# Kernel optimization log

Measured on AMD Instinct MI355X. Metric: run time of the kernel, lower is better.

Reference implementation:

```python
import jax, jax.numpy as jnp
import numpy as np

# ---- static config (matches init_kwargs) ----
B, CIN, H, W = 32, 64, 32, 32
CO, K, G, PAD = 64, 7, 8, 3
R_RAMP = 3.0            # ramp size R
Z_INIT = 4.0            # initial adaptive-span value
MAXSZ = W // 2          # adaptive_mask max_size = image_size/2 = 16
CPG = CO // G           # channels per group


def _unfold(t, k):
    # torch x.unfold(2,k,1).unfold(3,k,1): [B,C,Hp,Wp] -> [B,C,Ho,Wo,kh,kw]
    ho = t.shape[2] - k + 1
    wo = t.shape[3] - k + 1
    return jnp.stack(
        [jnp.stack([t[:, :, i:i + ho, j:j + wo] for j in range(k)], axis=-1)
         for i in range(k)], axis=-2)


def _adaptive_mask(current_val):
    # AdaptiveMask.forward applied to [B,G,CPG,H,W]; x.shape[-1] == W.
    # one_d_mask[g, i] is the soft value written on 'ring' i (rows i and W-1-i,
    # columns spanning the ring interval) of a WxW mask.
    template = jnp.linspace(1.0 - MAXSZ, 0.0, MAXSZ)            # [MAXSZ]
    om = (template[None, :] + current_val * MAXSZ) / R_RAMP + 1.0
    om = jnp.clip(om, 0.0, 1.0)                                  # [G, MAXSZ]
    # (slice [-(W//2):] is identity since MAXSZ == W//2)
    i = jnp.arange(W)
    r = jnp.minimum(i, W - 1 - i)                                # ring index per row
    top = i <= (W - 1 - i)
    lo = jnp.where(top, r, r + 1)    # bottom row of ring misses its leftmost col
    hi = W - 1 - r
    c = jnp.arange(W)
    in_ring = (c[None, :] >= lo[:, None]) & (c[None, :] <= hi[:, None])  # [W,W]
    vals = om[:, r]                                              # [G, W]
    return jnp.where(in_ring[None, :, :], vals[:, :, None], 1.0)  # [G,W,W]


def setup_inputs() -> dict:
    key = jax.random.key(0)
    ks = jax.random.split(key, 6)
    x = jax.random.normal(ks[0], (B, CIN, H, W), dtype=jnp.float32)
    fan_out_std = np.sqrt(2.0 / CO).astype(np.float32)  # kaiming fan_out, 1x1 conv
    w_q = jax.random.normal(ks[1], (CO, CIN), dtype=jnp.float32) * fan_out_std
    w_k = jax.random.normal(ks[2], (CO, CIN), dtype=jnp.float32) * fan_out_std
    w_v = jax.random.normal(ks[3], (CO, CIN), dtype=jnp.float32) * fan_out_std
    rel_h = jax.random.normal(ks[4], (CO // 2, 1, 1, K, 1), dtype=jnp.float32)
    rel_w = jax.random.normal(ks[5], (CO // 2, 1, 1, 1, K), dtype=jnp.float32)
    current_val = jnp.full((G, 1), Z_INIT, dtype=jnp.float32)
    return {"x": x, "w_q": w_q, "w_k": w_k, "w_v": w_v,
            "rel_h": rel_h, "rel_w": rel_w, "current_val": current_val}


def reference(x, w_q, w_k, w_v, rel_h, rel_w, current_val):
    q = jnp.einsum('bchw,oc->bohw', x, w_q)                       # [B,CO,H,W]
    xp = jnp.pad(x, ((0, 0), (0, 0), (PAD, PAD), (PAD, PAD)))
    k = jnp.einsum('bchw,oc->bohw', xp, w_k)
    v = jnp.einsum('bchw,oc->bohw', xp, w_v)
    k = _unfold(k, K)                                             # [B,CO,H,W,K,K]
    v = _unfold(v, K)
    k_h, k_w = jnp.split(k, 2, axis=1)
    k = jnp.concatenate([k_h + rel_h, k_w + rel_w], axis=1)
    k = k.reshape(B, G, CPG, H, W, K * K)
    v = v.reshape(B, G, CPG, H, W, K * K)
    q = q.reshape(B, G, CPG, H, W, 1)
    scores = jnp.sum(q * k, axis=2)                               # [B,G,H,W,K*K]
    attn = jax.nn.softmax(scores, axis=-1)
    out = jnp.sum(attn[:, :, None] * v, axis=-1)                  # [B,G,CPG,H,W]
    mask = _adaptive_mask(current_val)                            # [G,W,W]
    return out * mask[None, :, None, :, :]
```

## Files before the change

kernel.cpp:

```cpp
#include <hip/hip_runtime.h>

#define BB    32
#define CINc  64
#define HHc   32
#define WWc   32
#define COc   64
#define KSc   7
#define GGc   8
#define PADc  3
#define CPGc  8
#define NPIX  (HHc * WWc)

typedef _Float16 half2v __attribute__((ext_vector_type(2)));

#if defined(__has_builtin)
#if __has_builtin(__builtin_amdgcn_fdot2)
#define HAVE_FDOT2 1
#endif
#endif

__global__ __launch_bounds__(1024, 4) void fused_kernel(
    const float* __restrict__ x,
    const float* __restrict__ wq,
    const float* __restrict__ wk,
    const float* __restrict__ wv,
    const float* __restrict__ rel_h,
    const float* __restrict__ rel_w,
    const float* __restrict__ cv,
    float* __restrict__ out)
{
    __shared__ __attribute__((aligned(16))) float4 kpl[NPIX];
    __shared__ __attribute__((aligned(16))) float4 vpl0[NPIX];
    __shared__ __attribute__((aligned(16))) float4 vpl1[NPIX];

    const int bi  = blockIdx.x;
    const int xcd = bi & 7;
    const int t   = bi >> 3;
    const int im  = t & 3;
    const int g   = t >> 2;
    const int b   = im * 8 + xcd;
    const int o0  = g * CPGc;
    const int tid = threadIdx.x;
    const int w   = tid & 31;
    const int h   = tid >> 5;

    const float* xb = x + (size_t)b * CINc * NPIX;
    const float* xp = xb + tid;

    float ak[CPGc], av[CPGc], aq[CPGc];
#pragma unroll
    for (int oi = 0; oi < CPGc; ++oi) { ak[oi] = 0.f; av[oi] = 0.f; aq[oi] = 0.f; }

    for (int c0 = 0; c0 < CINc; c0 += 8) {
        float xv[8];
#pragma unroll
        for (int jj = 0; jj < 8; ++jj)
            xv[jj] = xp[(c0 + jj) * NPIX];
#pragma unroll
        for (int oi = 0; oi < CPGc; ++oi) {
            const float* wkr = wk + (o0 + oi) * CINc + c0;
            const float* wvr = wv + (o0 + oi) * CINc + c0;
            const float* wqr = wq + (o0 + oi) * CINc + c0;
#pragma unroll
            for (int jj = 0; jj < 8; ++jj) {
                ak[oi] = fmaf(xv[jj], wkr[jj], ak[oi]);
                av[oi] = fmaf(xv[jj], wvr[jj], av[oi]);
                aq[oi] = fmaf(xv[jj], wqr[jj], aq[oi]);
            }
        }
    }

    {
        float4 kst;
        half2v* kp = (half2v*)&kst;
#pragma unroll
        for (int jj = 0; jj < 4; ++jj)
            kp[jj] = half2v{(_Float16)ak[2 * jj], (_Float16)ak[2 * jj + 1]};
        kpl[tid]  = kst;
        vpl0[tid] = (float4){av[0], av[1], av[2], av[3]};
        vpl1[tid] = (float4){av[4], av[5], av[6], av[7]};
    }

#if HAVE_FDOT2
    half2v q2[4];
#pragma unroll
    for (int jj = 0; jj < 4; ++jj)
        q2[jj] = half2v{(_Float16)aq[2 * jj], (_Float16)aq[2 * jj + 1]};
#endif

    const bool use_h = (g < 4);
    const float* relp = use_h ? (rel_h + o0 * KSc) : (rel_w + (o0 - 32) * KSc);
    float qrel[KSc];
#pragma unroll
    for (int tt = 0; tt < KSc; ++tt) {
        float s = 0.f;
#pragma unroll
        for (int oi = 0; oi < CPGc; ++oi)
            s = fmaf(aq[oi], relp[oi * KSc + tt], s);
        qrel[tt] = s;
    }

    __syncthreads();

    int  xcl[KSc];
    bool xin[KSc];
#pragma unroll
    for (int kj = 0; kj < KSc; ++kj) {
        const int xx = w + kj - PADc;
        xin[kj] = (xx >= 0) && (xx < WWc);
        xcl[kj] = min(max(xx, 0), WWc - 1);
    }

    float den = 0.f;
    float acc[CPGc];
#pragma unroll
    for (int oi = 0; oi < CPGc; ++oi) acc[oi] = 0.f;

#pragma unroll
    for (int ki = 0; ki < KSc; ++ki) {
        const int y   = h + ki - PADc;
        const bool yin = (y >= 0) && (y < HHc);
        const int base = min(max(y, 0), HHc - 1) * WWc;
#pragma unroll
        for (int kj = 0; kj < KSc; ++kj) {
            const int p = base + xcl[kj];
            const float4 kraw = kpl[p];
            const float4 v0   = vpl0[p];
            const float4 v1   = vpl1[p];
            const bool in = yin && xin[kj];

            float d = 0.f;
#if HAVE_FDOT2
            const half2v* kh = (const half2v*)&kraw;
            d = __builtin_amdgcn_fdot2(q2[0], kh[0], d, false);
            d = __builtin_amdgcn_fdot2(q2[1], kh[1], d, false);
            d = __builtin_amdgcn_fdot2(q2[2], kh[2], d, false);
            d = __builtin_amdgcn_fdot2(q2[3], kh[3], d, false);
#else
            const half2v* kh = (const half2v*)&kraw;
#pragma unroll
            for (int jj = 0; jj < 4; ++jj) {
                d = fmaf(aq[2 * jj],     (float)kh[jj].x, d);
                d = fmaf(aq[2 * jj + 1], (float)kh[jj].y, d);
            }
#endif
            const float s = (use_h ? qrel[ki] : qrel[kj]) + (in ? d : 0.f);
            const float e = __expf(s);
            den += e;
            const float ev = in ? e : 0.f;
            acc[0] = fmaf(ev, v0.x, acc[0]); acc[1] = fmaf(ev, v0.y, acc[1]);
            acc[2] = fmaf(ev, v0.z, acc[2]); acc[3] = fmaf(ev, v0.w, acc[3]);
            acc[4] = fmaf(ev, v1.x, acc[4]); acc[5] = fmaf(ev, v1.y, acc[5]);
            acc[6] = fmaf(ev, v1.z, acc[6]); acc[7] = fmaf(ev, v1.w, acc[7]);
        }
    }

    const int  r  = min(h, HHc - 1 - h);
    const int  lo = (h <= HHc - 1 - h) ? r : r + 1;
    const int  hi = HHc - 1 - r;
    const bool in_ring = (w >= lo) && (w <= hi);
    const float cvg = cv[g];
    float om = ((float)r - 15.0f + cvg * 16.0f) * (1.0f / 3.0f) + 1.0f;
    om = fminf(fmaxf(om, 0.0f), 1.0f);
    const float maskv = in_ring ? om : 1.0f;
    const float scale = maskv / den;

    float* ob = out + ((size_t)b * COc + o0) * NPIX + tid;
#pragma unroll
    for (int oi = 0; oi < CPGc; ++oi)
        ob[(size_t)oi * NPIX] = acc[oi] * scale;
}

extern "C" void kernel_launch(void* const* d_in, const int* in_sizes, int n_in,
                              void* d_out, int out_size, void* d_ws, size_t ws_size,
                              hipStream_t stream) {
    const float* x     = (const float*)d_in[0];
    const float* wq    = (const float*)d_in[1];
    const float* wk    = (const float*)d_in[2];
    const float* wv    = (const float*)d_in[3];
    const float* rel_h = (const float*)d_in[4];
    const float* rel_w = (const float*)d_in[5];
    const float* cv    = (const float*)d_in[6];
    float* out = (float*)d_out;

    fused_kernel<<<256, 1024, 0, stream>>>(x, wq, wk, wv, rel_h, rel_w, cv, out);
}
```

Baseline: 103.7 us.

## Compute QKV 1x1 projections with fp16 MFMA instead of scalar FMAs

Replaces the per-thread scalar FMA loop for the q/k/v 1x1 convolutions with MFMA 16x16x32 fp16 instructions. Each wave computes 64 pixels, with K and V packed into one 16-column B tile and Q in a second tile. Results are scattered through shared memory, which needs a new Q buffer and an extra LDS round trip before the attention loop. This removes the heavy FMA work of the projection phase, at the cost of fp16 rounding of x, the weights and Q, and of scattered sub-word LDS stores.

```diff
diff --git a/kernel.cpp b/kernel.cpp
--- a/kernel.cpp
+++ b/kernel.cpp
@@ -11,7 +11,9 @@
 #define CPGc  8
 #define NPIX  (HHc * WWc)
 
-typedef _Float16 half2v __attribute__((ext_vector_type(2)));
+typedef _Float16 h8    __attribute__((ext_vector_type(8)));
+typedef _Float16 h2    __attribute__((ext_vector_type(2)));
+typedef float    f32x4 __attribute__((ext_vector_type(4)));
 
 #if defined(__has_builtin)
 #if __has_builtin(__builtin_amdgcn_fdot2)
@@ -29,9 +31,10 @@
     const float* __restrict__ cv,
     float* __restrict__ out)
 {
-    __shared__ __attribute__((aligned(16))) float4 kpl[NPIX];
-    __shared__ __attribute__((aligned(16))) float4 vpl0[NPIX];
-    __shared__ __attribute__((aligned(16))) float4 vpl1[NPIX];
+    __shared__ __attribute__((aligned(16))) f32x4 kplv[NPIX];
+    __shared__ __attribute__((aligned(16))) f32x4 vpl0[NPIX];
+    __shared__ __attribute__((aligned(16))) f32x4 vpl1[NPIX];
+    __shared__ __attribute__((aligned(16))) f32x4 qplv[NPIX];
 
     const int bi  = blockIdx.x;
     const int xcd = bi & 7;
@@ -44,49 +47,82 @@
     const int w   = tid & 31;
     const int h   = tid >> 5;
 
+    const int lane = tid & 63;
+    const int wp   = (tid >> 6) << 6;
+    const int an   = lane & 15;
+    const int quad = lane >> 4;
+
     const float* xb = x + (size_t)b * CINc * NPIX;
-    const float* xp = xb + tid;
-
-    float ak[CPGc], av[CPGc], aq[CPGc];
-#pragma unroll
-    for (int oi = 0; oi < CPGc; ++oi) { ak[oi] = 0.f; av[oi] = 0.f; aq[oi] = 0.f; }
-
-    for (int c0 = 0; c0 < CINc; c0 += 8) {
-        float xv[8];
-#pragma unroll
-        for (int jj = 0; jj < 8; ++jj)
-            xv[jj] = xp[(c0 + jj) * NPIX];
-#pragma unroll
-        for (int oi = 0; oi < CPGc; ++oi) {
-            const float* wkr = wk + (o0 + oi) * CINc + c0;
-            const float* wvr = wv + (o0 + oi) * CINc + c0;
-            const float* wqr = wq + (o0 + oi) * CINc + c0;
+
+    h8 bf[2][2];
+    {
+        const float* br0 = (an < 8) ? (wk + (o0 + an) * CINc)
+                                    : (wv + (o0 + an - 8) * CINc);
+        const float* br1 = wq + (o0 + ((an < 8) ? an : 0)) * CINc;
+#pragma unroll
+        for (int ks = 0; ks < 2; ++ks) {
+            const int c0 = ks * 32 + quad * 8;
 #pragma unroll
             for (int jj = 0; jj < 8; ++jj) {
-                ak[oi] = fmaf(xv[jj], wkr[jj], ak[oi]);
-                av[oi] = fmaf(xv[jj], wvr[jj], av[oi]);
-                aq[oi] = fmaf(xv[jj], wqr[jj], aq[oi]);
+                bf[0][ks][jj] = (_Float16)br0[c0 + jj];
+                bf[1][ks][jj] = (_Float16)br1[c0 + jj];
             }
         }
     }
 
+    f32x4 acc0[4], acc1[4];
+#pragma unroll
+    for (int m = 0; m < 4; ++m) { acc0[m] = (f32x4)0.f; acc1[m] = (f32x4)0.f; }
+
+#pragma unroll
+    for (int m = 0; m < 4; ++m) {
+        const float* xpx = xb + wp + m * 16 + an;
+#pragma unroll
+        for (int ks = 0; ks < 2; ++ks) {
+            const int c0 = ks * 32 + quad * 8;
+            h8 a;
+#pragma unroll
+            for (int jj = 0; jj < 8; ++jj)
+                a[jj] = (_Float16)xpx[(c0 + jj) * NPIX];
+            acc0[m] = __builtin_amdgcn_mfma_f32_16x16x32_f16(a, bf[0][ks], acc0[m], 0, 0, 0);
+            acc1[m] = __builtin_amdgcn_mfma_f32_16x16x32_f16(a, bf[1][ks], acc1[m], 0, 0, 0);
+        }
+    }
+
     {
-        float4 kst;
-        half2v* kp = (half2v*)&kst;
-#pragma unroll
-        for (int jj = 0; jj < 4; ++jj)
-            kp[jj] = half2v{(_Float16)ak[2 * jj], (_Float16)ak[2 * jj + 1]};
-        kpl[tid]  = kst;
-        vpl0[tid] = (float4){av[0], av[1], av[2], av[3]};
-        vpl1[tid] = (float4){av[4], av[5], av[6], av[7]};
-    }
-
-#if HAVE_FDOT2
-    half2v q2[4];
-#pragma unroll
-    for (int jj = 0; jj < 4; ++jj)
-        q2[jj] = half2v{(_Float16)aq[2 * jj], (_Float16)aq[2 * jj + 1]};
-#endif
+        _Float16* kp16 = (_Float16*)kplv;
+        _Float16* qp16 = (_Float16*)qplv;
+        float*    v0f  = (float*)vpl0;
+        float*    v1f  = (float*)vpl1;
+#pragma unroll
+        for (int m = 0; m < 4; ++m) {
+#pragma unroll
+            for (int r = 0; r < 4; ++r) {
+                const int pix = wp + m * 16 + quad * 4 + r;
+                const float d0 = acc0[m][r];
+                if (an < 8) {
+                    kp16[pix * 8 + an] = (_Float16)d0;
+                    qp16[pix * 8 + an] = (_Float16)acc1[m][r];
+                } else {
+                    const int c = an - 8;
+                    if (c < 4) v0f[pix * 4 + c]       = d0;
+                    else       v1f[pix * 4 + (c - 4)] = d0;
+                }
+            }
+        }
+    }
+
+    __syncthreads();
+
+    f32x4 qraw = qplv[tid];
+    const h2* qh = (const h2*)&qraw;
+    h2 q2[4] = {qh[0], qh[1], qh[2], qh[3]};
+    float qf[CPGc];
+#pragma unroll
+    for (int jj = 0; jj < 4; ++jj) {
+        qf[2 * jj]     = (float)q2[jj].x;
+        qf[2 * jj + 1] = (float)q2[jj].y;
+    }
 
     const bool use_h = (g < 4);
     const float* relp = use_h ? (rel_h + o0 * KSc) : (rel_w + (o0 - 32) * KSc);
@@ -96,11 +132,9 @@
         float s = 0.f;
 #pragma unroll
         for (int oi = 0; oi < CPGc; ++oi)
-            s = fmaf(aq[oi], relp[oi * KSc + tt], s);
+            s = fmaf(qf[oi], relp[oi * KSc + tt], s);
         qrel[tt] = s;
     }
-
-    __syncthreads();
 
     int  xcl[KSc];
     bool xin[KSc];
@@ -118,30 +152,30 @@
 
 #pragma unroll
     for (int ki = 0; ki < KSc; ++ki) {
-        const int y   = h + ki - PADc;
+        const int y    = h + ki - PADc;
         const bool yin = (y >= 0) && (y < HHc);
         const int base = min(max(y, 0), HHc - 1) * WWc;
 #pragma unroll
         for (int kj = 0; kj < KSc; ++kj) {
             const int p = base + xcl[kj];
-            const float4 kraw = kpl[p];
-            const float4 v0   = vpl0[p];
-            const float4 v1   = vpl1[p];
+            const f32x4 kraw = kplv[p];
+            const f32x4 v0   = vpl0[p];
+            const f32x4 v1   = vpl1[p];
             const bool in = yin && xin[kj];
 
             float d = 0.f;
 #if HAVE_FDOT2
-            const half2v* kh = (const half2v*)&kraw;
+            const h2* kh = (const h2*)&kraw;
             d = __builtin_amdgcn_fdot2(q2[0], kh[0], d, false);
             d = __builtin_amdgcn_fdot2(q2[1], kh[1], d, false);
             d = __builtin_amdgcn_fdot2(q2[2], kh[2], d, false);
             d = __builtin_amdgcn_fdot2(q2[3], kh[3], d, false);
 #else
-            const half2v* kh = (const half2v*)&kraw;
+            const h2* kh = (const h2*)&kraw;
 #pragma unroll
             for (int jj = 0; jj < 4; ++jj) {
-                d = fmaf(aq[2 * jj],     (float)kh[jj].x, d);
-                d = fmaf(aq[2 * jj + 1], (float)kh[jj].y, d);
+                d = fmaf(qf[2 * jj],     (float)kh[jj].x, d);
+                d = fmaf(qf[2 * jj + 1], (float)kh[jj].y, d);
             }
 #endif
             const float s = (use_h ? qrel[ki] : qrel[kj]) + (in ? d : 0.f);
```

Measured after the change: 87.52 us. 15.6% less time.
